# Optimization experiments

Hardware: AMD Instinct MI355X
Metric: run time of the kernel (lower is better)

## Reference

```python
import jax, jax.numpy as jnp
import numpy as np


def setup_inputs() -> dict:
    key = jax.random.key(0)
    k1, k2, k3 = jax.random.split(key, 3)
    B, L = 1024, 256
    preds = jax.random.normal(k1, (B, L), dtype=jnp.float32)
    targets = jax.random.randint(k2, (B, L), 0, 2, dtype=jnp.int32)
    mask = jax.random.randint(k3, (B, L), 0, 2, dtype=jnp.int32)
    return {"preds": preds, "targets": targets, "mask": mask}


def reference(preds, targets, mask):
    # preds: [B, L] float scores; targets: [B, L] 0/1 relevance; mask: [B, L] 0/1 valid.
    B, L = preds.shape
    t = targets.astype(preds.dtype)
    m = mask.astype(jnp.int32)
    # Full pairwise matrices; the original loop materializes exactly the i<j half,
    # which we select with an upper-triangular mask instead of per-i slices/concat.
    diff = preds[:, :, None] - preds[:, None, :]          # [B, L, L] score deltas
    tdiff = t[:, :, None] - t[:, None, :]                 # [B, L, L] label deltas (+-1 or 0)
    pmask = (m[:, :, None] & m[:, None, :]).astype(preds.dtype)  # [B, L, L] both valid
    tri = jnp.triu(jnp.ones((L, L), dtype=bool), k=1)     # pairs with i < j
    loss_mat = jax.nn.log_sigmoid(diff * tdiff) * (tdiff * pmask) ** 2
    loss = -jnp.sum(jnp.where(tri[None, :, :], loss_mat, jnp.zeros((), preds.dtype)))
    return loss
```

## Files before the change

kernel.cpp:

```cpp
#include <hip/hip_runtime.h>


#define BATCH 1024
#define LEN   256
#define LN2f   0.6931471805599453f
#define LOG2Ef 1.4426950408889634f

__global__ __launch_bounds__(256) void bpr_partial_kernel(
    const float* __restrict__ preds,
    const int*   __restrict__ targets,
    const int*   __restrict__ mask,
    float*       __restrict__ partial)
{
    __shared__ float spos[LEN];
    __shared__ float sneg[LEN];
    __shared__ int   wcp[4], wcn[4];
    __shared__ float wpart[4];

    const int b    = blockIdx.x;
    const int tid  = threadIdx.x;
    const int wid  = tid >> 6;
    const int lane = tid & 63;

    const float p = preds[b * LEN + tid] * LOG2Ef;
    const int   t = targets[b * LEN + tid];
    const int   m = mask[b * LEN + tid];

    const bool ispos = (m != 0) && (t != 0);
    const bool isneg = (m != 0) && (t == 0);

    const unsigned long long bp = __ballot(ispos);
    const unsigned long long bn = __ballot(isneg);
    if (lane == 0) { wcp[wid] = __popcll(bp); wcn[wid] = __popcll(bn); }
    __syncthreads();

    int opos = 0, oneg = 0;
    for (int w = 0; w < wid; ++w) { opos += wcp[w]; oneg += wcn[w]; }
    const int np = wcp[0] + wcp[1] + wcp[2] + wcp[3];
    const int nn = wcn[0] + wcn[1] + wcn[2] + wcn[3];

    const unsigned long long below = (1ull << lane) - 1ull;
    if (ispos) spos[opos + __popcll(bp & below)] = p;
    if (isneg) sneg[oneg + __popcll(bn & below)] = p;
    __syncthreads();

    float acc = 0.0f;
    for (int i = lane; i < np; i += 64) {
        const float yi = spos[i];
        for (int j = wid; j < nn; j += 4) {
            const float y = yi - sneg[j];
            const float e = __builtin_amdgcn_exp2f(-fabsf(y));
            const float l = __builtin_amdgcn_logf(1.0f + e);
            acc += fminf(y, 0.0f) - l;
        }
    }

    for (int off = 32; off > 0; off >>= 1)
        acc += __shfl_down(acc, off, 64);
    if (lane == 0) wpart[wid] = acc;
    __syncthreads();
    if (tid == 0)
        partial[b] = wpart[0] + wpart[1] + wpart[2] + wpart[3];
}

__global__ __launch_bounds__(256) void bpr_reduce_kernel(
    const float* __restrict__ partial,
    float*       __restrict__ out)
{
    const int i = threadIdx.x;
    float acc = 0.0f;
    #pragma unroll
    for (int k = i; k < BATCH; k += 256)
        acc += partial[k];

    for (int off = 32; off > 0; off >>= 1)
        acc += __shfl_down(acc, off, 64);

    __shared__ float wpart[4];
    if ((i & 63) == 0) wpart[i >> 6] = acc;
    __syncthreads();
    if (i == 0)
        out[0] = -LN2f * (wpart[0] + wpart[1] + wpart[2] + wpart[3]);
}

extern "C" void kernel_launch(void* const* d_in, const int* in_sizes, int n_in,
                              void* d_out, int out_size, void* d_ws, size_t ws_size,
                              hipStream_t stream) {
    const float* preds   = (const float*)d_in[0];
    const int*   targets = (const int*)d_in[1];
    const int*   mask    = (const int*)d_in[2];
    float* out     = (float*)d_out;
    float* partial = (float*)d_ws;

    bpr_partial_kernel<<<BATCH, 256, 0, stream>>>(preds, targets, mask, partial);
    bpr_reduce_kernel<<<1, 256, 0, stream>>>(partial, out);
}
```

Before: 12.21 us.

## Map one row per wavefront with vectorized loads and wave-local compaction

Each 256-thread block now processes four rows, one per wavefront. Each lane loads four elements as float4/int4 and compacts positives and negatives using wave-local ballots, with no cross-wave count exchange. The pair loop covers all negatives in one wave with an unrolled inner loop, and each wave writes its own partial directly, removing block-level reduction syncs. This trades the intra-row split across waves for per-row wave independence, which may increase per-wave imbalance across rows.

```diff
diff --git a/kernel.cpp b/kernel.cpp
--- a/kernel.cpp
+++ b/kernel.cpp
@@ -3,6 +3,8 @@
 
 #define BATCH 1024
 #define LEN   256
+#define RPB   4
+#define NBLK  (BATCH / RPB)
 #define LN2f   0.6931471805599453f
 #define LOG2Ef 1.4426950408889634f
 
@@ -12,43 +14,44 @@
     const int*   __restrict__ mask,
     float*       __restrict__ partial)
 {
-    __shared__ float spos[LEN];
-    __shared__ float sneg[LEN];
-    __shared__ int   wcp[4], wcn[4];
-    __shared__ float wpart[4];
+    __shared__ float spos[RPB][LEN];
+    __shared__ float sneg[RPB][LEN];
 
-    const int b    = blockIdx.x;
     const int tid  = threadIdx.x;
     const int wid  = tid >> 6;
     const int lane = tid & 63;
+    const int row  = blockIdx.x * RPB + wid;
+    const int base = row * LEN;
 
-    const float p = preds[b * LEN + tid] * LOG2Ef;
-    const int   t = targets[b * LEN + tid];
-    const int   m = mask[b * LEN + tid];
+    const float4 p4 = *reinterpret_cast<const float4*>(preds   + base + lane * 4);
+    const int4   t4 = *reinterpret_cast<const int4*>(targets + base + lane * 4);
+    const int4   m4 = *reinterpret_cast<const int4*>(mask    + base + lane * 4);
 
-    const bool ispos = (m != 0) && (t != 0);
-    const bool isneg = (m != 0) && (t == 0);
+    const float pv[4] = { p4.x * LOG2Ef, p4.y * LOG2Ef, p4.z * LOG2Ef, p4.w * LOG2Ef };
+    const int   tv[4] = { t4.x, t4.y, t4.z, t4.w };
+    const int   mv[4] = { m4.x, m4.y, m4.z, m4.w };
 
-    const unsigned long long bp = __ballot(ispos);
-    const unsigned long long bn = __ballot(isneg);
-    if (lane == 0) { wcp[wid] = __popcll(bp); wcn[wid] = __popcll(bn); }
-    __syncthreads();
-
-    int opos = 0, oneg = 0;
-    for (int w = 0; w < wid; ++w) { opos += wcp[w]; oneg += wcn[w]; }
-    const int np = wcp[0] + wcp[1] + wcp[2] + wcp[3];
-    const int nn = wcn[0] + wcn[1] + wcn[2] + wcn[3];
-
+    int np = 0, nn = 0;
     const unsigned long long below = (1ull << lane) - 1ull;
-    if (ispos) spos[opos + __popcll(bp & below)] = p;
-    if (isneg) sneg[oneg + __popcll(bn & below)] = p;
+    #pragma unroll
+    for (int s = 0; s < 4; ++s) {
+        const bool ispos = (mv[s] != 0) && (tv[s] != 0);
+        const bool isneg = (mv[s] != 0) && (tv[s] == 0);
+        const unsigned long long bp = __ballot(ispos);
+        const unsigned long long bn = __ballot(isneg);
+        if (ispos) spos[wid][np + __popcll(bp & below)] = pv[s];
+        if (isneg) sneg[wid][nn + __popcll(bn & below)] = pv[s];
+        np += (int)__popcll(bp);
+        nn += (int)__popcll(bn);
+    }
     __syncthreads();
 
     float acc = 0.0f;
-    for (int i = lane; i < np; i += 64) {
-        const float yi = spos[i];
-        for (int j = wid; j < nn; j += 4) {
-            const float y = yi - sneg[j];
+    for (int ip = lane; ip < np; ip += 64) {
+        const float yi = spos[wid][ip];
+        #pragma unroll 4
+        for (int jn = 0; jn < nn; ++jn) {
+            const float y = yi - sneg[wid][jn];
             const float e = __builtin_amdgcn_exp2f(-fabsf(y));
             const float l = __builtin_amdgcn_logf(1.0f + e);
             acc += fminf(y, 0.0f) - l;
@@ -57,10 +60,8 @@
 
     for (int off = 32; off > 0; off >>= 1)
         acc += __shfl_down(acc, off, 64);
-    if (lane == 0) wpart[wid] = acc;
-    __syncthreads();
-    if (tid == 0)
-        partial[b] = wpart[0] + wpart[1] + wpart[2] + wpart[3];
+    if (lane == 0)
+        partial[row] = acc;
 }
 
 __global__ __launch_bounds__(256) void bpr_reduce_kernel(
@@ -92,6 +93,6 @@
     float* out     = (float*)d_out;
     float* partial = (float*)d_ws;
 
-    bpr_partial_kernel<<<BATCH, 256, 0, stream>>>(preds, targets, mask, partial);
+    bpr_partial_kernel<<<NBLK, 256, 0, stream>>>(preds, targets, mask, partial);
     bpr_reduce_kernel<<<1, 256, 0, stream>>>(partial, out);
 }
```

Measured after the change: 13.26 us. +8.7%, slower.
